# Kernel tuning notes

Measured on AMD Instinct MI355X. Metric: run time of the kernel, lower is better.

## Reference

```python
import jax, jax.numpy as jnp
import numpy as np

B_SZ, L_SEQ, H_CH, N_ST = 8, 4096, 256, 64


def setup_inputs() -> dict:
    key = jax.random.key(0)
    ks = jax.random.split(key, 12)
    rn = lambda k, s, sc=1.0: jax.random.normal(k, s, jnp.float32) * sc
    inp = {
        'x': rn(ks[0], (B_SZ, L_SEQ, H_CH)),
        # stable DPLR spectrum: Re(Lambda) < 0, HiPPO-like imaginary ladder
        'Lambda_re': -(jnp.abs(rn(ks[1], (N_ST,))) + 0.1),
        'Lambda_im': jnp.pi * jnp.arange(N_ST, dtype=jnp.float32),
        'P_re': rn(ks[2], (N_ST,), N_ST ** -0.5),
        'P_im': rn(ks[3], (N_ST,), N_ST ** -0.5),
        'Q_re': rn(ks[4], (N_ST,), N_ST ** -0.5),
        'Q_im': rn(ks[5], (N_ST,), N_ST ** -0.5),
        'B_re': rn(ks[6], (N_ST,), N_ST ** -0.5),
        'B_im': rn(ks[7], (N_ST,), N_ST ** -0.5),
        'C_re': rn(ks[8], (H_CH, N_ST), N_ST ** -0.5),
        'C_im': rn(ks[9], (H_CH, N_ST), N_ST ** -0.5),
        'step': jnp.ones((1,), jnp.float32) * 1e-3,
        'D': jnp.zeros((1,), jnp.float32),
        'W_fc': rn(ks[10], (H_CH, H_CH), H_CH ** -0.5),
        'b_fc': jnp.zeros((H_CH,), jnp.float32),
        'ln_g': jnp.ones((H_CH,), jnp.float32),
        'ln_b': jnp.zeros((H_CH,), jnp.float32),
    }
    return inp


def _dplr_kernel(Lambda_re, Lambda_im, P_re, P_im, Q_re, Q_im, B_re, B_im, C_re, C_im, step, L):
    # S4 DPLR generating function evaluated at the L roots of unity (torch_get_K_derta).
    Lam = (Lambda_re + 1j * Lambda_im).astype(jnp.complex64)  # (N,)
    Pc = (P_re + 1j * P_im).astype(jnp.complex64)
    Qc = (Q_re + 1j * Q_im).astype(jnp.complex64)
    Bc = (B_re + 1j * B_im).astype(jnp.complex64)
    Cc = (C_re + 1j * C_im).astype(jnp.complex64)  # (H, N)
    k = jnp.arange(L, dtype=jnp.float32)
    Omega = jnp.exp((-2j * jnp.pi) * (k / L)).astype(jnp.complex64)  # (L,)
    c = 2.0 / (1.0 + Omega)
    g = (2.0 / step[0]) * (1.0 - Omega) / (1.0 + Omega)  # bilinear transform points, (L,)
    inv = 1.0 / (g[:, None] - Lam[None, :])  # Cauchy matrix, (L, N)
    k00 = jnp.einsum('hn,ln->hl', Cc * Bc[None, :], inv)  # (H, L)
    k01 = jnp.einsum('hn,ln->hl', Cc * Pc[None, :], inv)
    k10 = jnp.einsum('n,ln->l', Qc * Bc, inv)  # (L,)
    k11 = jnp.einsum('n,ln->l', Qc * Pc, inv)
    atRoots = c[None, :] * (k00 - k01 * (k10 / (1.0 + k11))[None, :])  # Woodbury correction
    K = jnp.fft.ifft(atRoots, axis=-1).real  # (H, L)
    return K.astype(jnp.float32)


def reference(x, Lambda_re, Lambda_im, P_re, P_im, Q_re, Q_im, B_re, B_im, C_re, C_im, step, D, W_fc, b_fc, ln_g, ln_b):
    Bsz, L, H = x.shape
    step = jnp.maximum(step, 1e-6)
    K = _dplr_kernel(Lambda_re, Lambda_im, P_re, P_im, Q_re, Q_im, B_re, B_im, C_re, C_im, step, L)  # (H, L)
    # causal FFT convolution per channel (torch_convolution with fft=True)
    n = 2 * L
    Kf = jnp.fft.rfft(K, n=n, axis=-1)           # (H, F)
    uf = jnp.fft.rfft(x, n=n, axis=1)            # (B, F, H)
    h1 = jnp.fft.irfft(uf * Kf.T[None], n=n, axis=1)[:, :L, :]
    y1 = jax.nn.gelu(h1 + D * x, approximate=False)  # mult_activation='gelu'
    y2 = jax.nn.gelu(y1 @ W_fc.T + b_fc, approximate=False)  # fc + final_act
    y2 = y2 + x  # skip
    mu = jnp.mean(y2, axis=-1, keepdims=True)
    var = jnp.var(y2, axis=-1, keepdims=True)
    y = (y2 - mu) / jnp.sqrt(var + 1e-5) * ln_g + ln_b  # LayerNorm; dropout p=0
    h_ratio = jnp.max(jnp.abs(y), axis=1) / (jnp.max(jnp.abs(x), axis=1) + 1e-6)  # (B, H)
    return y, h_ratio
```

## Files before the change

### kernel.cpp

```cpp
#include <hip/hip_runtime.h>
#include <math.h>

typedef float2 cf;
typedef __attribute__((ext_vector_type(8))) short bf16x8;
typedef __attribute__((ext_vector_type(4))) float f32x4;

__device__ __forceinline__ cf cmk(float x, float y){ cf r; r.x=x; r.y=y; return r; }
__device__ __forceinline__ cf cml(cf a, cf b){ return cmk(a.x*b.x - a.y*b.y, a.x*b.y + a.y*b.x); }
__device__ __forceinline__ cf cad(cf a, cf b){ return cmk(a.x+b.x, a.y+b.y); }
__device__ __forceinline__ cf csb(cf a, cf b){ return cmk(a.x-b.x, a.y-b.y); }
__device__ __forceinline__ cf cjg(cf a){ return cmk(a.x, -a.y); }
__device__ __forceinline__ cf crcp(cf d){ float r = 1.0f/(d.x*d.x + d.y*d.y); return cmk(d.x*r, -d.y*r); }
__device__ __forceinline__ cf cdv(cf n, cf d){ return cml(n, crcp(d)); }
__device__ __forceinline__ float geluf(float z){ return 0.5f*z*(1.0f + erff(z*0.70710678118654752f)); }

__device__ __forceinline__ cf twid(float f, float sign){
  float h = f * 0.5f;
  float s = __builtin_amdgcn_sinf(h);
  float c0 = __builtin_amdgcn_cosf(h);
  return cmk(c0, sign * s);
}

__device__ __forceinline__ cf shflx(cf v, int m){
  return cmk(__shfl_xor(v.x, m), __shfl_xor(v.y, m));
}

__device__ __forceinline__ void bfsplit(float v, ushort* h, ushort* l){
  unsigned u = __float_as_uint(v);
  unsigned hr = (u + 0x7FFFu + ((u >> 16) & 1u)) & 0xFFFF0000u;
  *h = (ushort)(hr >> 16);
  float lv = v - __uint_as_float(hr);
  unsigned u2 = __float_as_uint(lv);
  *l = (ushort)((u2 + 0x7FFFu + ((u2 >> 16) & 1u)) >> 16);
}

__device__ __forceinline__ void dif4q(cf& q0, cf& q1, cf& q2, cf& q3, cf w1, float sign){
  cf w2 = cml(w1, w1);
  cf a1 = cad(q0, q2);
  cf c1 = cml(csb(q0, q2), w1);
  cf b1 = cad(q1, q3);
  cf d1 = cml(csb(q1, q3), cmk(-sign*w1.y, sign*w1.x));
  q0 = cad(a1, b1);
  q1 = cml(csb(a1, b1), w2);
  q2 = cad(c1, d1);
  q3 = cml(csb(c1, d1), w2);
}
__device__ __forceinline__ void dit4q(cf& q0, cf& q1, cf& q2, cf& q3, cf w1, float sign){
  cf w2 = cml(w1, w1);
  cf t1 = cml(q1, w2);
  cf a1 = cad(q0, t1), b1 = csb(q0, t1);
  cf t2 = cml(q3, w2);
  cf c1 = cad(q2, t2), d1 = csb(q2, t2);
  cf v1 = cml(c1, w1);
  cf v2 = cml(d1, cmk(-sign*w1.y, sign*w1.x));
  q0 = cad(a1, v1);
  q2 = csb(a1, v1);
  q1 = cad(b1, v2);
  q3 = csb(b1, v2);
}

__device__ __forceinline__ int brev12(int x){ return (int)(__brev((unsigned)x) >> 20); }
__device__ __forceinline__ int brev13(int x){ return (int)(__brev((unsigned)x) >> 19); }
__device__ __forceinline__ int pidx(int n){ return n + 4*(n>>8); }

template<int N, int SSTART, int TP>
__device__ void fft_dif_r4(cf* __restrict__ a, float sign){
  #pragma unroll
  for (int s = SSTART; s >= 1; s >>= 2){
    __syncthreads();
    #pragma unroll
    for (int g = 0; g < (N >> 2) / TP; g++){
      int w = (int)threadIdx.x + g * TP;
      int j = w & (s - 1);
      int base = ((w & ~(s - 1)) << 2) | j;
      cf A0 = a[base], B0 = a[base + s], C0 = a[base + 2*s], D0 = a[base + 3*s];
      cf w1 = twid((float)j / (float)(2 * s), sign);
      cf w2 = cml(w1, w1);
      cf a1 = cad(A0, C0);
      cf c1 = cml(csb(A0, C0), w1);
      cf b1 = cad(B0, D0);
      cf d1 = cml(csb(B0, D0), cmk(-sign * w1.y, sign * w1.x));
      a[base]         = cad(a1, b1);
      a[base + s]     = cml(csb(a1, b1), w2);
      a[base + 2*s]   = cad(c1, d1);
      a[base + 3*s]   = cml(csb(c1, d1), w2);
    }
  }
  if constexpr ((__builtin_ctz(N) & 1) == 1){
    __syncthreads();
    #pragma unroll
    for (int g = 0; g < (N >> 1) / TP; g++){
      int w = (int)threadIdx.x + g * TP;
      int i = w << 1;
      cf u = a[i], v = a[i + 1];
      a[i] = cad(u, v);
      a[i + 1] = csb(u, v);
    }
  }
  __syncthreads();
}

template<int N, int TP>
__device__ void fft_dit_r4(cf* __restrict__ a, float sign){
  if constexpr ((__builtin_ctz(N) & 1) == 1){
    __syncthreads();
    #pragma unroll
    for (int g = 0; g < (N >> 1) / TP; g++){
      int w = (int)threadIdx.x + g * TP;
      int i = w << 1;
      cf u = a[i], v = a[i + 1];
      a[i] = cad(u, v);
      a[i + 1] = csb(u, v);
    }
  }
  constexpr int S0 = ((__builtin_ctz(N) & 1) == 1) ? 2 : 1;
  #pragma unroll
  for (int s = S0; s <= (N >> 2); s <<= 2){
    __syncthreads();
    #pragma unroll
    for (int g = 0; g < (N >> 2) / TP; g++){
      int w = (int)threadIdx.x + g * TP;
      int j = w & (s - 1);
      int base = ((w & ~(s - 1)) << 2) | j;
      cf A0 = a[base], B0 = a[base + s], C0 = a[base + 2*s], D0 = a[base + 3*s];
      cf w1 = twid((float)j / (float)(2 * s), sign);
      cf w2 = cml(w1, w1);
      cf t1 = cml(B0, w2);
      cf a1 = cad(A0, t1), b1 = csb(A0, t1);
      cf t2 = cml(D0, w2);
      cf c1 = cad(C0, t2), d1 = csb(C0, t2);
      cf v1 = cml(c1, w1);
      cf v2 = cml(d1, cmk(-sign * w1.y, sign * w1.x));
      a[base]         = cad(a1, v1);
      a[base + 2*s]   = csb(a1, v1);
      a[base + s]     = cad(b1, v2);
      a[base + 3*s]   = csb(b1, v2);
    }
  }
  __syncthreads();
}

template<int TP>
__device__ void dif8192_pad_stage(cf* __restrict__ a, float sign){
  __syncthreads();
  #pragma unroll
  for (int g = 0; g < 2048 / TP; g++){
    int w = (int)threadIdx.x + g * TP;
    cf A0 = a[w], B0 = a[w + 2048];
    cf w1 = twid((float)w * (1.0f / 4096.0f), sign);
    cf w2 = cml(w1, w1);
    cf c1 = cml(A0, w1);
    cf d1 = cml(B0, cmk(-sign * w1.y, sign * w1.x));
    a[w]        = cad(A0, B0);
    a[w + 2048] = cml(csb(A0, B0), w2);
    a[w + 4096] = cad(c1, d1);
    a[w + 6144] = cml(csb(c1, d1), w2);
  }
}

__global__ void k_init(unsigned* xmax, unsigned* ymax){
  int i = blockIdx.x * 256 + threadIdx.x;
  if (i < 2048){ xmax[i] = 0u; ymax[i] = 0u; }
}

__global__ __launch_bounds__(256) void k_transpose_x(const float* __restrict__ x,
                                                     float* __restrict__ xT,
                                                     unsigned* __restrict__ xmax){
  __shared__ float tile[64][65];
  __shared__ float red[64][4];
  int b = blockIdx.z;
  int t0 = blockIdx.x * 64;
  int h0 = blockIdx.y * 64;
  int hc = threadIdx.x & 63, tg = threadIdx.x >> 6;
  float pmax = 0.0f;
  #pragma unroll
  for (int q = 0; q < 16; q++){
    int tr = tg + q * 4;
    float v = x[((size_t)(b * 4096 + t0 + tr)) * 256 + h0 + hc];
    tile[tr][hc] = v;
    pmax = fmaxf(pmax, fabsf(v));
  }
  red[hc][tg] = pmax;
  __syncthreads();
  if (threadIdx.x < 64){
    float m = fmaxf(fmaxf(red[threadIdx.x][0], red[threadIdx.x][1]),
                    fmaxf(red[threadIdx.x][2], red[threadIdx.x][3]));
    atomicMax(&xmax[b * 256 + h0 + threadIdx.x], __float_as_uint(m));
  }
  #pragma unroll
  for (int q = 0; q < 16; q++){
    int hr = tg + q * 4;
    xT[((size_t)(b * 256 + h0 + hr)) * 4096 + t0 + hc] = tile[hc][hr];
  }
}

__global__ void k_wsplit(const float* __restrict__ W, ushort* __restrict__ Wh, ushort* __restrict__ Wl){
  int i = blockIdx.x * 256 + threadIdx.x;
  ushort h, l;
  bfsplit(W[i], &h, &l);
  Wh[i] = h; Wl[i] = l;
}

__global__ __launch_bounds__(256) void k_cauchy(
    const float* __restrict__ Lr, const float* __restrict__ Li,
    const float* __restrict__ Pr, const float* __restrict__ Pi,
    const float* __restrict__ Qr, const float* __restrict__ Qi,
    const float* __restrict__ Br, const float* __restrict__ Bi,
    const float* __restrict__ Cr, const float* __restrict__ Ci,
    const float* __restrict__ stepp, cf* __restrict__ A)
{
  __shared__ cf sLam[64], sB[64], sP[64], sQB[64], sQP[64];
  __shared__ cf sInv[64][16];
  __shared__ cf sWood[16], sC[16], sG[16];
  int tid = threadIdx.x;
  int l0 = blockIdx.x * 16;
  float stepv = fmaxf(stepp[0], 1e-6f);
  if (tid < 64){
    cf lam = cmk(Lr[tid], Li[tid]);
    cf b = cmk(Br[tid], Bi[tid]);
    cf p = cmk(Pr[tid], Pi[tid]);
    cf q = cmk(Qr[tid], Qi[tid]);
    sLam[tid] = lam; sB[tid] = b; sP[tid] = p;
    sQB[tid] = cml(q, b);
    sQP[tid] = cml(q, p);
  }
  __syncthreads();
  if (tid < 16){
    int l = l0 + tid;
    float ang = -6.2831855f * ((float)l * (1.0f / 4096.0f));
    cf Om = cmk(cosf(ang), sinf(ang));
    cf den = cmk(1.0f + Om.x, Om.y);
    cf num = cmk(1.0f - Om.x, -Om.y);
    cf rden = crcp(den);
    sC[tid] = cml(cmk(2.0f, 0.0f), rden);
    cf g = cml(num, rden);
    float sc = 2.0f / stepv;
    sG[tid] = cmk(g.x * sc, g.y * sc);
  }
  __syncthreads();
  for (int it = tid; it < 1024; it += 256){
    int n = it >> 4, ll = it & 15;
    sInv[n][ll] = crcp(csb(sG[ll], sLam[n]));
  }
  __syncthreads();
  if (tid < 16){
    cf k10 = cmk(0,0), k11 = cmk(0,0);
    for (int n = 0; n < 64; n++){
      k10 = cad(k10, cml(sQB[n], sInv[n][tid]));
      k11 = cad(k11, cml(sQP[n], sInv[n][tid]));
    }
    sWood[tid] = cdv(k10, cmk(1.0f + k11.x, k11.y));
  }
  __syncthreads();
  int h = tid;
  cf a0[16], a1[16];
  #pragma unroll
  for (int ll = 0; ll < 16; ll++){ a0[ll] = cmk(0,0); a1[ll] = cmk(0,0); }
  for (int n = 0; n < 64; n++){
    cf cc = cmk(Cr[h * 64 + n], Ci[h * 64 + n]);
    cf cb = cml(cc, sB[n]);
    cf cp = cml(cc, sP[n]);
    #pragma unroll
    for (int ll = 0; ll < 16; ll++){
      cf iv = sInv[n][ll];
      a0[ll] = cad(a0[ll], cml(cb, iv));
      a1[ll] = cad(a1[ll], cml(cp, iv));
    }
  }
  cf* dst = A + (size_t)h * 4096 + l0;
  #pragma unroll
  for (int ll = 0; ll < 16; ll++){
    dst[ll] = cml(sC[ll], csb(a0[ll], cml(a1[ll], sWood[ll])));
  }
}

__global__ __launch_bounds__(512) void k_kf(const cf* __restrict__ A, float4* __restrict__ Sab){
  extern __shared__ cf c[];
  int hp = blockIdx.x, tid = threadIdx.x;
  const cf* a1p = A + (size_t)(2 * hp) * 4096;
  const cf* a2p = a1p + 4096;
  for (int l = tid; l < 4096; l += 512){
    int r = brev12(l);
    cf u = a1p[l], w = a2p[l];
    c[r] = cmk(u.x - w.y, u.y + w.x);
  }
  fft_dit_r4<4096, 512>(c, 1.0f);
  float k1[8], k2[8];
  #pragma unroll
  for (int q = 0; q < 8; q++){
    cf w = c[tid + q * 512];
    k1[q] = w.x * (1.0f / 4096.0f);
    k2[q] = w.y * (1.0f / 4096.0f);
  }
  __syncthreads();
  #pragma unroll
  for (int q = 0; q < 8; q++) c[tid + q * 512] = cmk(k1[q], k2[q]);
  dif8192_pad_stage<512>(c, -1.0f);
  fft_dif_r4<8192, 512, 512>(c, -1.0f);
  float4* rec = Sab + (size_t)hp * 4097;
  const float sc = 0.5f * 0.5f * (1.0f / 8192.0f);
  #pragma unroll
  for (int q8 = 0; q8 < 8; q8++){
    int t = tid + 512 * q8;
    int p = t << 1;
    int k = brev13(p);
    int qq = brev13((8192 - k) & 8191);
    cf Zp = c[p], Zq = c[qq];
    float K1x = (Zp.x + Zq.x), K1y = (Zp.y - Zq.y);
    float dx  = (Zp.x - Zq.x), dy  = (Zp.y + Zq.y);
    float K2x = dy, K2y = -dx;
    rec[t] = make_float4((K1x + K2x) * sc, (K1y + K2y) * sc,
                         (K1x - K2x) * sc, (K1y - K2y) * sc);
  }
  if (tid == 0){
    cf Z1 = c[1];
    float K1x = 2.0f * Z1.x, K2x = 2.0f * Z1.y;
    rec[4096] = make_float4((K1x + K2x) * sc, 0.0f, (K1x - K2x) * sc, 0.0f);
  }
}

__global__ __launch_bounds__(512) void k_conv(const float* __restrict__ xT,
                                              const float4* __restrict__ Sab,
                                              const float* __restrict__ Dp,
                                              ushort* __restrict__ y1h,
                                              ushort* __restrict__ y1l){
  __shared__ cf c[8320];
  int blk = blockIdx.x;
  int b = blk >> 7, hp = blk & 127;
  int t = threadIdx.x;
  int a = t >> 5, cl = t & 31;
  const float* xs1 = xT + ((size_t)(b * 256 + 2 * hp)) * 4096;
  const float* xs2 = xs1 + 4096;
  cf v[16];
  #pragma unroll
  for (int r = 0; r < 8; r++){
    int n = t + 512 * r;
    v[r] = cmk(xs1[n], xs2[n]);
  }
  #pragma unroll
  for (int r = 0; r < 8; r++)
    v[r + 8] = cml(v[r], twid((float)(t + 512 * r) * (1.0f / 4096.0f), -1.0f));
  #pragma unroll
  for (int h = 0; h < 16; h += 8){
    #pragma unroll
    for (int r0 = 0; r0 < 2; r0++){
      cf w1 = twid((float)(t + 512 * r0) * (1.0f / 2048.0f), -1.0f);
      dif4q(v[h + r0], v[h + r0 + 2], v[h + r0 + 4], v[h + r0 + 6], w1, -1.0f);
    }
  }
  {
    cf tw = twid((float)t * (1.0f / 512.0f), -1.0f);
    #pragma unroll
    for (int r = 0; r < 16; r += 2){
      cf lo = cad(v[r], v[r + 1]);
      cf hi = cml(csb(v[r], v[r + 1]), tw);
      v[r] = lo; v[r + 1] = hi;
    }
  }
  __syncthreads();
  #pragma unroll
  for (int r = 0; r < 16; r++) c[pidx(t + 512 * r)] = v[r];
  __syncthreads();
  #pragma unroll
  for (int u = 0; u < 16; u++) v[u] = c[pidx(a * 512 + u * 32 + cl)];
  #pragma unroll
  for (int u0 = 0; u0 < 4; u0++){
    cf w1 = twid((float)(u0 * 32 + cl) * (1.0f / 256.0f), -1.0f);
    dif4q(v[u0], v[u0 + 4], v[u0 + 8], v[u0 + 12], w1, -1.0f);
  }
  {
    cf w1 = twid((float)cl * (1.0f / 64.0f), -1.0f);
    #pragma unroll
    for (int g = 0; g < 16; g += 4)
      dif4q(v[g], v[g + 1], v[g + 2], v[g + 3], w1, -1.0f);
  }
  #pragma unroll
  for (int m = 16; m >= 2; m >>= 1){
    bool hb = (cl & m) != 0;
    cf tw = twid((float)(cl & (m - 1)) * (1.0f / (float)m), -1.0f);
    #pragma unroll
    for (int u = 0; u < 16; u++){
      cf o = shflx(v[u], m);
      v[u] = hb ? cml(csb(o, v[u]), tw) : cad(v[u], o);
    }
  }
  {
    bool hb = (cl & 1) != 0;
    #pragma unroll
    for (int u = 0; u < 16; u++){
      cf o = shflx(v[u], 1);
      v[u] = hb ? csb(o, v[u]) : cad(v[u], o);
    }
  }
  #pragma unroll
  for (int u = 0; u < 16; u++) c[pidx(a * 512 + u * 32 + cl)] = v[u];
  __syncthreads();
  {
    const float4* rec = Sab + (size_t)hp * 4097;
    #pragma unroll
    for (int q8 = 0; q8 < 8; q8++){
      int th = t + 512 * q8;
      int p = th << 1;
      int k = brev13(p);
      int qq = brev13((8192 - k) & 8191);
      int pi = pidx(p), qi = pidx(qq);
      cf Zp = c[pi], Zq = c[qi];
      float4 r0 = rec[th];
      cf Sap = cmk(r0.x, r0.y), Sbp = cmk(r0.z, r0.w);
      c[pi] = cad(cml(Zp, Sap), cml(cjg(Zq), Sbp));
      c[qi] = cad(cml(Zq, cjg(Sap)), cml(cjg(Zp), cjg(Sbp)));
    }
    if (t == 0){
      float4 e = rec[4096];
      cf Z1 = c[pidx(1)];
      c[pidx(1)] = cad(cml(Z1, cmk(e.x, e.y)), cml(cjg(Z1), cmk(e.z, e.w)));
    }
  }
  __syncthreads();
  #pragma unroll
  for (int u = 0; u < 16; u++) v[u] = c[pidx(a * 512 + u * 32 + cl)];
  {
    bool hb = (cl & 1) != 0;
    #pragma unroll
    for (int u = 0; u < 16; u++){
      cf o = shflx(v[u], 1);
      v[u] = hb ? csb(o, v[u]) : cad(v[u], o);
    }
  }
  #pragma unroll
  for (int m = 2; m <= 16; m <<= 1){
    bool hb = (cl & m) != 0;
    cf w = twid((float)(cl & (m - 1)) * (1.0f / (float)m), 1.0f);
    #pragma unroll
    for (int u = 0; u < 16; u++){
      cf o = shflx(v[u], m);
      cf whv = cml(w, hb ? v[u] : o);
      v[u] = hb ? csb(o, whv) : cad(v[u], whv);
    }
  }
  {
    cf w1 = twid((float)cl * (1.0f / 64.0f), 1.0f);
    #pragma unroll
    for (int g = 0; g < 16; g += 4)
      dit4q(v[g], v[g + 1], v[g + 2], v[g + 3], w1, 1.0f);
  }
  #pragma unroll
  for (int u0 = 0; u0 < 4; u0++){
    cf w1 = twid((float)(u0 * 32 + cl) * (1.0f / 256.0f), 1.0f);
    dit4q(v[u0], v[u0 + 4], v[u0 + 8], v[u0 + 12], w1, 1.0f);
  }
  #pragma unroll
  for (int u = 0; u < 16; u++) c[pidx(a * 512 + u * 32 + cl)] = v[u];
  __syncthreads();
  #pragma unroll
  for (int r = 0; r < 16; r++) v[r] = c[pidx(t + 512 * r)];
  {
    cf tw = twid((float)t * (1.0f / 512.0f), 1.0f);
    #pragma unroll
    for (int r = 0; r < 16; r += 2){
      cf tb = cml(v[r + 1], tw);
      cf a0 = v[r];
      v[r] = cad(a0, tb);
      v[r + 1] = csb(a0, tb);
    }
  }
  #pragma unroll
  for (int h = 0; h < 16; h += 8){
    #pragma unroll
    for (int r0 = 0; r0 < 2; r0++){
      cf w1 = twid((float)(t + 512 * r0) * (1.0f / 2048.0f), 1.0f);
      dit4q(v[h + r0], v[h + r0 + 2], v[h + r0 + 4], v[h + r0 + 6], w1, 1.0f);
    }
  }
  float Dv = Dp[0];
  size_t base = ((size_t)(b * 256 + 2 * hp)) * 4096;
  #pragma unroll
  for (int r = 0; r < 8; r++){
    int n = t + 512 * r;
    cf w = cad(v[r], cml(v[r + 8], twid((float)n * (1.0f / 4096.0f), 1.0f)));
    float z1 = geluf(fmaf(Dv, xs1[n], w.x));
    float z2 = geluf(fmaf(Dv, xs2[n], w.y));
    ushort h0, l0, h1u, l1;
    bfsplit(z1, &h0, &l0);
    bfsplit(z2, &h1u, &l1);
    y1h[base + n] = h0;         y1l[base + n] = l0;
    y1h[base + 4096 + n] = h1u; y1l[base + 4096 + n] = l1;
  }
}

__global__ __launch_bounds__(256, 3) void k_gemm_ln(
    const ushort* __restrict__ y1h, const ushort* __restrict__ y1l,
    const ushort* __restrict__ Wh, const ushort* __restrict__ Wl,
    const float* __restrict__ bfc, const float* __restrict__ x,
    const float* __restrict__ lng, const float* __restrict__ lnb,
    float* __restrict__ yout, unsigned* __restrict__ ymax)
{
  __shared__ ushort sY[2][64 * 40];
  __shared__ float red1[64][4], red2[64][4];
  int tid = threadIdx.x;
  int l = tid & 63;
  int w = tid >> 6;
  int blk = blockIdx.x;
  int b = blk >> 6;
  int t0 = (blk & 63) * 64;
  int g = l >> 4, cc = l & 15;

  f32x4 acc[4][4];
  #pragma unroll
  for (int m = 0; m < 4; m++)
    #pragma unroll
    for (int n = 0; n < 4; n++)
      acc[m][n] = (f32x4){0.0f, 0.0f, 0.0f, 0.0f};

  int kk = tid >> 3, ts = (tid & 7) * 8;

  #pragma unroll 1
  for (int kc = 0; kc < 256; kc += 32){
    __syncthreads();
    {
      size_t gb = ((size_t)(b * 256 + kc + kk)) * 4096 + t0 + ts;
      float4 vh = *(const float4*)(y1h + gb);
      float4 vl = *(const float4*)(y1l + gb);
      const ushort* ph = (const ushort*)&vh;
      const ushort* pl = (const ushort*)&vl;
      int kblk = kk >> 3, kin = kk & 7;
      #pragma unroll
      for (int e = 0; e < 8; e++){
        int t = ts + e;
        int idx = t * 40 + ((kblk ^ ((t >> 3) & 3)) << 3) + kin;
        sY[0][idx] = ph[e];
        sY[1][idx] = pl[e];
      }
    }
    __syncthreads();
    bf16x8 afh[4], afl[4];
    #pragma unroll
    for (int m = 0; m < 4; m++){
      int t = m * 16 + cc;
      int idx = t * 40 + ((g ^ ((t >> 3) & 3)) << 3);
      afh[m] = *(bf16x8*)&sY[0][idx];
      afl[m] = *(bf16x8*)&sY[1][idx];
    }
    #pragma unroll
    for (int n = 0; n < 4; n++){
      size_t wj = (size_t)(w * 64 + n * 16 + cc) * 256 + kc + g * 8;
      bf16x8 bh = *(const bf16x8*)(Wh + wj);
      bf16x8 bl = *(const bf16x8*)(Wl + wj);
      #pragma unroll
      for (int m = 0; m < 4; m++){
        acc[m][n] = __builtin_amdgcn_mfma_f32_16x16x32_bf16(afh[m], bh, acc[m][n], 0, 0, 0);
        acc[m][n] = __builtin_amdgcn_mfma_f32_16x16x32_bf16(afh[m], bl, acc[m][n], 0, 0, 0);
        acc[m][n] = __builtin_amdgcn_mfma_f32_16x16x32_bf16(afl[m], bh, acc[m][n], 0, 0, 0);
      }
    }
  }

  float bj[4], gj[4], lj[4];
  #pragma unroll
  for (int n = 0; n < 4; n++){
    int j = w * 64 + n * 16 + cc;
    bj[n] = bfc[j]; gj[n] = lng[j]; lj[n] = lnb[j];
  }
  #pragma unroll
  for (int m = 0; m < 4; m++){
    #pragma unroll
    for (int r = 0; r < 4; r++){
      int tl = m * 16 + g * 4 + r;
      size_t rowb = ((size_t)(b * 4096 + t0 + tl)) * 256;
      float ss = 0.0f, sq = 0.0f;
      #pragma unroll
      for (int n = 0; n < 4; n++){
        float z = geluf(acc[m][n][r] + bj[n]) + x[rowb + w * 64 + n * 16 + cc];
        acc[m][n][r] = z;
        ss += z; sq = fmaf(z, z, sq);
      }
      #pragma unroll
      for (int msk = 1; msk < 16; msk <<= 1){
        ss += __shfl_xor(ss, msk);
        sq += __shfl_xor(sq, msk);
      }
      if (cc == 0){ red1[tl][w] = ss; red2[tl][w] = sq; }
    }
  }
  __syncthreads();
  float jm[4] = {0.0f, 0.0f, 0.0f, 0.0f};
  #pragma unroll
  for (int m = 0; m < 4; m++){
    #pragma unroll
    for (int r = 0; r < 4; r++){
      int tl = m * 16 + g * 4 + r;
      float ts1 = red1[tl][0] + red1[tl][1] + red1[tl][2] + red1[tl][3];
      float ts2 = red2[tl][0] + red2[tl][1] + red2[tl][2] + red2[tl][3];
      float mu = ts1 * (1.0f / 256.0f);
      float var = ts2 * (1.0f / 256.0f) - mu * mu;
      float rstd = rsqrtf(var + 1e-5f);
      size_t rowb = ((size_t)(b * 4096 + t0 + tl)) * 256;
      #pragma unroll
      for (int n = 0; n < 4; n++){
        float yv = (acc[m][n][r] - mu) * rstd * gj[n] + lj[n];
        yout[rowb + w * 64 + n * 16 + cc] = yv;
        jm[n] = fmaxf(jm[n], fabsf(yv));
      }
    }
  }
  #pragma unroll
  for (int n = 0; n < 4; n++){
    jm[n] = fmaxf(jm[n], __shfl_xor(jm[n], 16));
    jm[n] = fmaxf(jm[n], __shfl_xor(jm[n], 32));
  }
  if (g == 0){
    #pragma unroll
    for (int n = 0; n < 4; n++)
      atomicMax(&ymax[b * 256 + w * 64 + n * 16 + cc], __float_as_uint(jm[n]));
  }
}

__global__ void k_ratio(const unsigned* __restrict__ ymax, const unsigned* __restrict__ xmax,
                        float* __restrict__ out){
  int i = blockIdx.x * 256 + threadIdx.x;
  if (i < 2048){
    float ym = __uint_as_float(ymax[i]);
    float xm = __uint_as_float(xmax[i]);
    out[8388608 + i] = ym / (xm + 1e-6f);
  }
}

extern "C" void kernel_launch(void* const* d_in, const int* in_sizes, int n_in,
                              void* d_out, int out_size, void* d_ws, size_t ws_size,
                              hipStream_t stream)
{
  const float* x    = (const float*)d_in[0];
  const float* Lr   = (const float*)d_in[1];
  const float* Li   = (const float*)d_in[2];
  const float* Pr   = (const float*)d_in[3];
  const float* Pi   = (const float*)d_in[4];
  const float* Qr   = (const float*)d_in[5];
  const float* Qi   = (const float*)d_in[6];
  const float* Br   = (const float*)d_in[7];
  const float* Bi   = (const float*)d_in[8];
  const float* Cr   = (const float*)d_in[9];
  const float* Ci   = (const float*)d_in[10];
  const float* stp  = (const float*)d_in[11];
  const float* Dp   = (const float*)d_in[12];
  const float* Wfc  = (const float*)d_in[13];
  const float* bfc  = (const float*)d_in[14];
  const float* lng  = (const float*)d_in[15];
  const float* lnb  = (const float*)d_in[16];

  char* ws = (char*)d_ws;
  float*    xT   = (float*)(ws);
  float4*   Sab  = (float4*)(ws + ((size_t)32 << 20));
  cf*       A    = (cf*)(ws + ((size_t)41 << 20));
  ushort*   y1h  = (ushort*)(ws + ((size_t)41 << 20));
  ushort*   y1l  = (ushort*)(ws + ((size_t)57 << 20));
  ushort*   Wh   = (ushort*)(ws + ((size_t)73 << 20));
  ushort*   Wl   = (ushort*)(ws + ((size_t)73 << 20) + (128u << 10));
  unsigned* xmax = (unsigned*)(ws + ((size_t)73 << 20) + (256u << 10));
  unsigned* ymax = xmax + 2048;

  k_init<<<8, 256, 0, stream>>>(xmax, ymax);
  dim3 gt(64, 4, 8);
  k_transpose_x<<<gt, 256, 0, stream>>>(x, xT, xmax);
  k_wsplit<<<256, 256, 0, stream>>>(Wfc, Wh, Wl);
  k_cauchy<<<256, 256, 0, stream>>>(Lr, Li, Pr, Pi, Qr, Qi, Br, Bi, Cr, Ci, stp, A);
  k_kf<<<128, 512, 65536, stream>>>(A, Sab);
  k_conv<<<1024, 512, 0, stream>>>(xT, Sab, Dp, y1h, y1l);
  k_gemm_ln<<<512, 256, 0, stream>>>(y1h, y1l, Wh, Wl, bfc, x, lng, lnb, (float*)d_out, ymax);
  k_ratio<<<8, 256, 0, stream>>>(ymax, xmax, (float*)d_out);
}
```

Measured before the change: 213.8 us.

## Restructure conv FFT to 256 threads with 32 points each and LDS radix-4 stages

The 8192-point FFT convolution kernel now runs with 256 threads per block, each holding 32 complex values instead of 16. The warp-shuffle radix-2 stages are replaced by an extra shared-memory transpose pass that does radix-4 stages in registers, with twiddle-free radix-4 butterflies and vectorized float4 LDS accesses. This cuts shuffle traffic and twiddle computation per element. In exchange it adds more LDS round trips and barriers, and it doubles register pressure per thread, which can lower occupancy.

```diff
diff --git a/kernel.cpp b/kernel.cpp
--- a/kernel.cpp
+++ b/kernel.cpp
@@ -19,10 +19,6 @@
   float s = __builtin_amdgcn_sinf(h);
   float c0 = __builtin_amdgcn_cosf(h);
   return cmk(c0, sign * s);
-}
-
-__device__ __forceinline__ cf shflx(cf v, int m){
-  return cmk(__shfl_xor(v.x, m), __shfl_xor(v.y, m));
 }
 
 __device__ __forceinline__ void bfsplit(float v, ushort* h, ushort* l){
@@ -57,6 +53,20 @@
   q2 = csb(a1, v1);
   q1 = cad(b1, v2);
   q3 = csb(b1, v2);
+}
+__device__ __forceinline__ void dif4q0(cf& q0, cf& q1, cf& q2, cf& q3, float sign){
+  cf a1 = cad(q0, q2), c1 = csb(q0, q2);
+  cf b1 = cad(q1, q3), d0 = csb(q1, q3);
+  cf d1 = cmk(-sign*d0.y, sign*d0.x);
+  q0 = cad(a1, b1); q1 = csb(a1, b1);
+  q2 = cad(c1, d1); q3 = csb(c1, d1);
+}
+__device__ __forceinline__ void dit4q0(cf& q0, cf& q1, cf& q2, cf& q3, float sign){
+  cf a1 = cad(q0, q1), b1 = csb(q0, q1);
+  cf c1 = cad(q2, q3), d0 = csb(q2, q3);
+  cf v2 = cmk(-sign*d0.y, sign*d0.x);
+  q0 = cad(a1, c1); q2 = csb(a1, c1);
+  q1 = cad(b1, v2); q3 = csb(b1, v2);
 }
 
 __device__ __forceinline__ int brev12(int x){ return (int)(__brev((unsigned)x) >> 20); }
@@ -319,87 +329,95 @@
   }
 }
 
-__global__ __launch_bounds__(512) void k_conv(const float* __restrict__ xT,
+__global__ __launch_bounds__(256) void k_conv(const float* __restrict__ xT,
                                               const float4* __restrict__ Sab,
                                               const float* __restrict__ Dp,
                                               ushort* __restrict__ y1h,
                                               ushort* __restrict__ y1l){
-  __shared__ cf c[8320];
+  __shared__ __align__(16) cf c[8320];
   int blk = blockIdx.x;
   int b = blk >> 7, hp = blk & 127;
   int t = threadIdx.x;
-  int a = t >> 5, cl = t & 31;
+  int lo4 = t & 15, hiT = t >> 4;
+  int base0 = lo4 + ((hiT << 1) << 8);
+  int base1 = lo4 + ((((hiT << 1) | 1)) << 8);
+  int cb0 = pidx((t << 1) << 4);
+  int cb1 = pidx(((t << 1) | 1) << 4);
   const float* xs1 = xT + ((size_t)(b * 256 + 2 * hp)) * 4096;
   const float* xs2 = xs1 + 4096;
-  cf v[16];
-  #pragma unroll
-  for (int r = 0; r < 8; r++){
-    int n = t + 512 * r;
+  cf v[32];
+  #pragma unroll
+  for (int r = 0; r < 16; r++){
+    int n = t + 256 * r;
     v[r] = cmk(xs1[n], xs2[n]);
   }
   #pragma unroll
-  for (int r = 0; r < 8; r++)
-    v[r + 8] = cml(v[r], twid((float)(t + 512 * r) * (1.0f / 4096.0f), -1.0f));
-  #pragma unroll
-  for (int h = 0; h < 16; h += 8){
-    #pragma unroll
-    for (int r0 = 0; r0 < 2; r0++){
-      cf w1 = twid((float)(t + 512 * r0) * (1.0f / 2048.0f), -1.0f);
-      dif4q(v[h + r0], v[h + r0 + 2], v[h + r0 + 4], v[h + r0 + 6], w1, -1.0f);
-    }
+  for (int r = 0; r < 16; r++)
+    v[r + 16] = cml(v[r], twid((float)(t + 256 * r) * (1.0f / 4096.0f), -1.0f));
+  #pragma unroll
+  for (int r0 = 0; r0 < 4; r0++){
+    cf w1 = twid((float)(t + 256 * r0) * (1.0f / 2048.0f), -1.0f);
+    dif4q(v[r0], v[r0 + 4], v[r0 + 8], v[r0 + 12], w1, -1.0f);
+    dif4q(v[16 + r0], v[16 + r0 + 4], v[16 + r0 + 8], v[16 + r0 + 12], w1, -1.0f);
   }
   {
-    cf tw = twid((float)t * (1.0f / 512.0f), -1.0f);
-    #pragma unroll
-    for (int r = 0; r < 16; r += 2){
-      cf lo = cad(v[r], v[r + 1]);
-      cf hi = cml(csb(v[r], v[r + 1]), tw);
-      v[r] = lo; v[r + 1] = hi;
-    }
-  }
-  __syncthreads();
-  #pragma unroll
-  for (int r = 0; r < 16; r++) c[pidx(t + 512 * r)] = v[r];
-  __syncthreads();
-  #pragma unroll
-  for (int u = 0; u < 16; u++) v[u] = c[pidx(a * 512 + u * 32 + cl)];
+    cf w1 = twid((float)t * (1.0f / 512.0f), -1.0f);
+    #pragma unroll
+    for (int g = 0; g < 32; g += 4)
+      dif4q(v[g], v[g + 1], v[g + 2], v[g + 3], w1, -1.0f);
+  }
+  #pragma unroll
+  for (int r = 0; r < 32; r++) c[pidx(t + 256 * r)] = v[r];
+  __syncthreads();
+  #pragma unroll
+  for (int u = 0; u < 16; u++){
+    v[u]      = c[pidx(base0 + (u << 4))];
+    v[16 + u] = c[pidx(base1 + (u << 4))];
+  }
   #pragma unroll
   for (int u0 = 0; u0 < 4; u0++){
-    cf w1 = twid((float)(u0 * 32 + cl) * (1.0f / 256.0f), -1.0f);
+    cf w1 = twid((float)(lo4 + (u0 << 4)) * (1.0f / 128.0f), -1.0f);
     dif4q(v[u0], v[u0 + 4], v[u0 + 8], v[u0 + 12], w1, -1.0f);
+    dif4q(v[16 + u0], v[16 + u0 + 4], v[16 + u0 + 8], v[16 + u0 + 12], w1, -1.0f);
   }
   {
-    cf w1 = twid((float)cl * (1.0f / 64.0f), -1.0f);
-    #pragma unroll
-    for (int g = 0; g < 16; g += 4)
+    cf w1 = twid((float)lo4 * (1.0f / 32.0f), -1.0f);
+    #pragma unroll
+    for (int g = 0; g < 32; g += 4)
       dif4q(v[g], v[g + 1], v[g + 2], v[g + 3], w1, -1.0f);
   }
   #pragma unroll
-  for (int m = 16; m >= 2; m >>= 1){
-    bool hb = (cl & m) != 0;
-    cf tw = twid((float)(cl & (m - 1)) * (1.0f / (float)m), -1.0f);
-    #pragma unroll
-    for (int u = 0; u < 16; u++){
-      cf o = shflx(v[u], m);
-      v[u] = hb ? cml(csb(o, v[u]), tw) : cad(v[u], o);
-    }
-  }
-  {
-    bool hb = (cl & 1) != 0;
-    #pragma unroll
-    for (int u = 0; u < 16; u++){
-      cf o = shflx(v[u], 1);
-      v[u] = hb ? csb(o, v[u]) : cad(v[u], o);
-    }
-  }
-  #pragma unroll
-  for (int u = 0; u < 16; u++) c[pidx(a * 512 + u * 32 + cl)] = v[u];
+  for (int u = 0; u < 16; u++){
+    c[pidx(base0 + (u << 4))] = v[u];
+    c[pidx(base1 + (u << 4))] = v[16 + u];
+  }
+  __syncthreads();
+  #pragma unroll
+  for (int k = 0; k < 8; k++){
+    float4 q0 = *(const float4*)&c[cb0 + 2 * k];
+    float4 q1 = *(const float4*)&c[cb1 + 2 * k];
+    v[2 * k]      = cmk(q0.x, q0.y); v[2 * k + 1]      = cmk(q0.z, q0.w);
+    v[16 + 2 * k] = cmk(q1.x, q1.y); v[16 + 2 * k + 1] = cmk(q1.z, q1.w);
+  }
+  #pragma unroll
+  for (int u0 = 0; u0 < 4; u0++){
+    cf w1 = twid((float)u0 * 0.125f, -1.0f);
+    dif4q(v[u0], v[u0 + 4], v[u0 + 8], v[u0 + 12], w1, -1.0f);
+    dif4q(v[16 + u0], v[16 + u0 + 4], v[16 + u0 + 8], v[16 + u0 + 12], w1, -1.0f);
+  }
+  #pragma unroll
+  for (int g = 0; g < 32; g += 4) dif4q0(v[g], v[g + 1], v[g + 2], v[g + 3], -1.0f);
+  #pragma unroll
+  for (int k = 0; k < 8; k++){
+    *(float4*)&c[cb0 + 2 * k] = make_float4(v[2*k].x, v[2*k].y, v[2*k+1].x, v[2*k+1].y);
+    *(float4*)&c[cb1 + 2 * k] = make_float4(v[16+2*k].x, v[16+2*k].y, v[16+2*k+1].x, v[16+2*k+1].y);
+  }
   __syncthreads();
   {
     const float4* rec = Sab + (size_t)hp * 4097;
     #pragma unroll
-    for (int q8 = 0; q8 < 8; q8++){
-      int th = t + 512 * q8;
+    for (int q8 = 0; q8 < 16; q8++){
+      int th = t + 256 * q8;
       int p = th << 1;
       int k = brev13(p);
       int qq = brev13((8192 - k) & 8191);
@@ -418,66 +436,69 @@
   }
   __syncthreads();
   #pragma unroll
-  for (int u = 0; u < 16; u++) v[u] = c[pidx(a * 512 + u * 32 + cl)];
+  for (int k = 0; k < 8; k++){
+    float4 q0 = *(const float4*)&c[cb0 + 2 * k];
+    float4 q1 = *(const float4*)&c[cb1 + 2 * k];
+    v[2 * k]      = cmk(q0.x, q0.y); v[2 * k + 1]      = cmk(q0.z, q0.w);
+    v[16 + 2 * k] = cmk(q1.x, q1.y); v[16 + 2 * k + 1] = cmk(q1.z, q1.w);
+  }
+  #pragma unroll
+  for (int g = 0; g < 32; g += 4) dit4q0(v[g], v[g + 1], v[g + 2], v[g + 3], 1.0f);
+  #pragma unroll
+  for (int u0 = 0; u0 < 4; u0++){
+    cf w1 = twid((float)u0 * 0.125f, 1.0f);
+    dit4q(v[u0], v[u0 + 4], v[u0 + 8], v[u0 + 12], w1, 1.0f);
+    dit4q(v[16 + u0], v[16 + u0 + 4], v[16 + u0 + 8], v[16 + u0 + 12], w1, 1.0f);
+  }
+  #pragma unroll
+  for (int k = 0; k < 8; k++){
+    *(float4*)&c[cb0 + 2 * k] = make_float4(v[2*k].x, v[2*k].y, v[2*k+1].x, v[2*k+1].y);
+    *(float4*)&c[cb1 + 2 * k] = make_float4(v[16+2*k].x, v[16+2*k].y, v[16+2*k+1].x, v[16+2*k+1].y);
+  }
+  __syncthreads();
+  #pragma unroll
+  for (int u = 0; u < 16; u++){
+    v[u]      = c[pidx(base0 + (u << 4))];
+    v[16 + u] = c[pidx(base1 + (u << 4))];
+  }
   {
-    bool hb = (cl & 1) != 0;
-    #pragma unroll
-    for (int u = 0; u < 16; u++){
-      cf o = shflx(v[u], 1);
-      v[u] = hb ? csb(o, v[u]) : cad(v[u], o);
-    }
-  }
-  #pragma unroll
-  for (int m = 2; m <= 16; m <<= 1){
-    bool hb = (cl & m) != 0;
-    cf w = twid((float)(cl & (m - 1)) * (1.0f / (float)m), 1.0f);
-    #pragma unroll
-    for (int u = 0; u < 16; u++){
-      cf o = shflx(v[u], m);
-      cf whv = cml(w, hb ? v[u] : o);
-      v[u] = hb ? csb(o, whv) : cad(v[u], whv);
-    }
-  }
+    cf w1 = twid((float)lo4 * (1.0f / 32.0f), 1.0f);
+    #pragma unroll
+    for (int g = 0; g < 32; g += 4)
+      dit4q(v[g], v[g + 1], v[g + 2], v[g + 3], w1, 1.0f);
+  }
+  #pragma unroll
+  for (int u0 = 0; u0 < 4; u0++){
+    cf w1 = twid((float)(lo4 + (u0 << 4)) * (1.0f / 128.0f), 1.0f);
+    dit4q(v[u0], v[u0 + 4], v[u0 + 8], v[u0 + 12], w1, 1.0f);
+    dit4q(v[16 + u0], v[16 + u0 + 4], v[16 + u0 + 8], v[16 + u0 + 12], w1, 1.0f);
+  }
+  #pragma unroll
+  for (int u = 0; u < 16; u++){
+    c[pidx(base0 + (u << 4))] = v[u];
+    c[pidx(base1 + (u << 4))] = v[16 + u];
+  }
+  __syncthreads();
+  #pragma unroll
+  for (int r = 0; r < 32; r++) v[r] = c[pidx(t + 256 * r)];
   {
-    cf w1 = twid((float)cl * (1.0f / 64.0f), 1.0f);
-    #pragma unroll
-    for (int g = 0; g < 16; g += 4)
+    cf w1 = twid((float)t * (1.0f / 512.0f), 1.0f);
+    #pragma unroll
+    for (int g = 0; g < 32; g += 4)
       dit4q(v[g], v[g + 1], v[g + 2], v[g + 3], w1, 1.0f);
   }
   #pragma unroll
-  for (int u0 = 0; u0 < 4; u0++){
-    cf w1 = twid((float)(u0 * 32 + cl) * (1.0f / 256.0f), 1.0f);
-    dit4q(v[u0], v[u0 + 4], v[u0 + 8], v[u0 + 12], w1, 1.0f);
-  }
-  #pragma unroll
-  for (int u = 0; u < 16; u++) c[pidx(a * 512 + u * 32 + cl)] = v[u];
-  __syncthreads();
-  #pragma unroll
-  for (int r = 0; r < 16; r++) v[r] = c[pidx(t + 512 * r)];
-  {
-    cf tw = twid((float)t * (1.0f / 512.0f), 1.0f);
-    #pragma unroll
-    for (int r = 0; r < 16; r += 2){
-      cf tb = cml(v[r + 1], tw);
-      cf a0 = v[r];
-      v[r] = cad(a0, tb);
-      v[r + 1] = csb(a0, tb);
-    }
-  }
-  #pragma unroll
-  for (int h = 0; h < 16; h += 8){
-    #pragma unroll
-    for (int r0 = 0; r0 < 2; r0++){
-      cf w1 = twid((float)(t + 512 * r0) * (1.0f / 2048.0f), 1.0f);
-      dit4q(v[h + r0], v[h + r0 + 2], v[h + r0 + 4], v[h + r0 + 6], w1, 1.0f);
-    }
+  for (int r0 = 0; r0 < 4; r0++){
+    cf w1 = twid((float)(t + 256 * r0) * (1.0f / 2048.0f), 1.0f);
+    dit4q(v[r0], v[r0 + 4], v[r0 + 8], v[r0 + 12], w1, 1.0f);
+    dit4q(v[16 + r0], v[16 + r0 + 4], v[16 + r0 + 8], v[16 + r0 + 12], w1, 1.0f);
   }
   float Dv = Dp[0];
   size_t base = ((size_t)(b * 256 + 2 * hp)) * 4096;
   #pragma unroll
-  for (int r = 0; r < 8; r++){
-    int n = t + 512 * r;
-    cf w = cad(v[r], cml(v[r + 8], twid((float)n * (1.0f / 4096.0f), 1.0f)));
+  for (int r = 0; r < 16; r++){
+    int n = t + 256 * r;
+    cf w = cad(v[r], cml(v[r + 16], twid((float)n * (1.0f / 4096.0f), 1.0f)));
     float z1 = geluf(fmaf(Dv, xs1[n], w.x));
     float z2 = geluf(fmaf(Dv, xs2[n], w.y));
     ushort h0, l0, h1u, l1;
@@ -664,7 +685,7 @@
   k_wsplit<<<256, 256, 0, stream>>>(Wfc, Wh, Wl);
   k_cauchy<<<256, 256, 0, stream>>>(Lr, Li, Pr, Pi, Qr, Qi, Br, Bi, Cr, Ci, stp, A);
   k_kf<<<128, 512, 65536, stream>>>(A, Sab);
-  k_conv<<<1024, 512, 0, stream>>>(xT, Sab, Dp, y1h, y1l);
+  k_conv<<<1024, 256, 0, stream>>>(xT, Sab, Dp, y1h, y1l);
   k_gemm_ln<<<512, 256, 0, stream>>>(y1h, y1l, Wh, Wl, bfc, x, lng, lnb, (float*)d_out, ymax);
   k_ratio<<<8, 256, 0, stream>>>(ymax, xmax, (float*)d_out);
 }
```

Result: no change. 215.3 us (+0.7%).
